# Kernel optimization log

Hardware: AMD Instinct MI355X
Metric: run time of the kernel (lower is better)

Reference implementation:

```python
import jax, jax.numpy as jnp
import numpy as np

B, S, D, H = 4, 2048, 1024, 16
DH = D // H  # head dim == module's 'scale'


def setup_inputs() -> dict:
    key = jax.random.key(0)
    ks = jax.random.split(key, 9)
    std = 1.0 / np.sqrt(D)
    return {
        "x": jax.random.normal(ks[0], (B, S, D), dtype=jnp.float32),
        "Wq": jax.random.normal(ks[1], (D, D), dtype=jnp.float32) * std,
        "bq": jax.random.normal(ks[2], (D,), dtype=jnp.float32) * std,
        "Wk": jax.random.normal(ks[3], (D, D), dtype=jnp.float32) * std,
        "bk": jax.random.normal(ks[4], (D,), dtype=jnp.float32) * std,
        "Wv": jax.random.normal(ks[5], (D, D), dtype=jnp.float32) * std,
        "bv": jax.random.normal(ks[6], (D,), dtype=jnp.float32) * std,
        "Wo": jax.random.normal(ks[7], (D, D), dtype=jnp.float32) * std,
        "bo": jax.random.normal(ks[8], (D,), dtype=jnp.float32) * std,
    }


def reference(x, Wq, bq, Wk, bk, Wv, bv, Wo, bo):
    b, s, d = x.shape
    # torch Linear: y = x @ W.T + b
    q = (x @ Wq.T + bq).reshape(b, s, H, DH).transpose(0, 2, 1, 3)  # [B,H,S,Dh]
    k = (x @ Wk.T + bk).reshape(b, s, H, DH).transpose(0, 2, 1, 3)
    v = (x @ Wv.T + bv).reshape(b, s, H, DH).transpose(0, 2, 1, 3)
    # scaled dot-product with causal mask (prefill: Tq == Tk, empty cache)
    scores = jnp.einsum("bhqd,bhkd->bhqk", q, k) / jnp.sqrt(
        jnp.asarray(DH, dtype=jnp.float32))
    causal = jnp.tril(jnp.ones((s, s), dtype=bool))  # [S,S]
    scores = jnp.where(causal, scores, jnp.asarray(-1e9, dtype=scores.dtype))
    attn = jax.nn.softmax(scores, axis=-1)
    out = jnp.einsum("bhqk,bhkd->bhqd", attn, v)  # [B,H,S,Dh]
    out = out.transpose(0, 2, 1, 3).reshape(b, s, d)
    return out @ Wo.T + bo
```

## Files before the change

kernel.cpp:

```cpp
#include <hip/hip_runtime.h>
#include <hip/hip_bf16.h>
#include <stdint.h>

#define NB 4
#define NS 2048
#define ND 1024
#define NH 16
#define NDH 64
#define NM (NB*NS)

typedef __attribute__((ext_vector_type(8))) short bf16x8;
typedef __attribute__((ext_vector_type(4))) float f32x4;
typedef __attribute__((ext_vector_type(16))) float f32x16;
typedef __attribute__((ext_vector_type(8))) unsigned short u16x8;

static __device__ __forceinline__ unsigned short f2bf(float f) {
  union { float f; unsigned u; } v; v.f = f;
  return (unsigned short)((v.u + 0x7FFFu + ((v.u >> 16) & 1u)) >> 16);
}

static __device__ __forceinline__ void gload_lds16(const void* g, void* l) {
  __builtin_amdgcn_global_load_lds(
      (__attribute__((address_space(1))) unsigned int*)(uintptr_t)g,
      (__attribute__((address_space(3))) unsigned int*)(uintptr_t)(size_t)(l),
      16, 0, 0);
}

static __device__ __forceinline__ unsigned cvtpk(float lo, float hi) {
  unsigned r;
  asm("v_cvt_pk_bf16_f32 %0, %1, %2" : "=v"(r) : "v"(lo), "v"(hi));
  return r;
}
static __device__ __forceinline__ void plswap(unsigned &a, unsigned &b) {
  asm("v_permlane32_swap_b32 %0, %1" : "+v"(a), "+v"(b));
}

__global__ void k_cvt(const float* __restrict__ src, unsigned short* __restrict__ dst, int n8) {
  int i = blockIdx.x * blockDim.x + threadIdx.x;
  if (i >= n8) return;
  const float4* s = (const float4*)src + (size_t)i * 2;
  float4 a = s[0], b = s[1];
  u16x8 o;
  o[0]=f2bf(a.x); o[1]=f2bf(a.y); o[2]=f2bf(a.z); o[3]=f2bf(a.w);
  o[4]=f2bf(b.x); o[5]=f2bf(b.y); o[6]=f2bf(b.z); o[7]=f2bf(b.w);
  *((u16x8*)dst + i) = o;
}

__global__ void k_cvtw(const float* __restrict__ s0, const float* __restrict__ s1,
                       const float* __restrict__ s2, const float* __restrict__ s3,
                       unsigned short* __restrict__ d0, unsigned short* __restrict__ d1,
                       unsigned short* __restrict__ d2, unsigned short* __restrict__ d3) {
  constexpr int NG = ND*ND/8;
  int i = blockIdx.x * blockDim.x + threadIdx.x;
  const int m = i / NG, j = i - m*NG;
  const float* src = m==0 ? s0 : (m==1 ? s1 : (m==2 ? s2 : s3));
  unsigned short* dst = m==0 ? d0 : (m==1 ? d1 : (m==2 ? d2 : d3));
  const float4* s = (const float4*)src + (size_t)j * 2;
  float4 a = s[0], b = s[1];
  u16x8 o;
  o[0]=f2bf(a.x); o[1]=f2bf(a.y); o[2]=f2bf(a.z); o[3]=f2bf(a.w);
  o[4]=f2bf(b.x); o[5]=f2bf(b.y); o[6]=f2bf(b.z); o[7]=f2bf(b.w);
  *((u16x8*)dst + j) = o;
}

__global__ __launch_bounds__(256)
void k_gemm_qkv(const unsigned short* __restrict__ A,
                const unsigned short* __restrict__ Wqp, const unsigned short* __restrict__ Wkp,
                const unsigned short* __restrict__ Wvp,
                const float* __restrict__ bqp, const float* __restrict__ bkp,
                const float* __restrict__ bvp,
                unsigned short* __restrict__ Qo, unsigned short* __restrict__ Ko,
                unsigned short* __restrict__ Vto, float qscale)
{
  constexpr int K = ND, BK = 32;
  __shared__ unsigned short Alds[128*BK];
  __shared__ unsigned short Blds[128*BK];
  const int bcf = blockIdx.x;
  const int mat = bcf >> 3, bc = bcf & 7;
  const unsigned short* W = mat==0 ? Wqp : (mat==1 ? Wkp : Wvp);
  const float* bias = mat==0 ? bqp : (mat==1 ? bkp : bvp);
  const float scale = mat==0 ? qscale : 1.0f;

  const int tid = threadIdx.x;
  const int wid = tid >> 6, lane = tid & 63;
  const int g = lane >> 4, lr = lane & 15;
  const int br = blockIdx.y;
  const int wr = (wid >> 1) << 6, wc = (wid & 1) << 6;

  f32x4 acc[4][4];
  #pragma unroll
  for (int m=0;m<4;m++)
    #pragma unroll
    for (int n=0;n<4;n++) acc[m][n] = f32x4{0.f,0.f,0.f,0.f};

  const unsigned short* Ab = A + (size_t)br*128*K;
  const unsigned short* Wb = W + (size_t)bc*128*K;
  const int r0 = tid >> 2, c0 = (tid & 3) * 8;
  const int r1 = (256 + tid) >> 2;

  for (int k0 = 0; k0 < K; k0 += BK) {
    gload_lds16(Ab + (size_t)r0*K + k0 + c0, &Alds[tid*8]);
    gload_lds16(Ab + (size_t)r1*K + k0 + c0, &Alds[(256+tid)*8]);
    gload_lds16(Wb + (size_t)r0*K + k0 + c0, &Blds[tid*8]);
    gload_lds16(Wb + (size_t)r1*K + k0 + c0, &Blds[(256+tid)*8]);
    __syncthreads();
    bf16x8 af[4], bfr[4];
    #pragma unroll
    for (int m=0;m<4;m++) af[m]  = *(const bf16x8*)&Alds[(wr + m*16 + lr)*BK + g*8];
    #pragma unroll
    for (int n=0;n<4;n++) bfr[n] = *(const bf16x8*)&Blds[(wc + n*16 + lr)*BK + g*8];
    #pragma unroll
    for (int m=0;m<4;m++)
      #pragma unroll
      for (int n=0;n<4;n++)
        acc[m][n] = __builtin_amdgcn_mfma_f32_16x16x32_bf16(af[m], bfr[n], acc[m][n], 0, 0, 0);
    __syncthreads();
  }

  #pragma unroll
  for (int m=0;m<4;m++) {
    const int rbase = br*128 + wr + m*16 + g*4;
    #pragma unroll
    for (int n=0;n<4;n++) {
      const int col = bc*128 + wc + n*16 + lr;
      const float bv = bias[col];
      #pragma unroll
      for (int j=0;j<4;j++) {
        const int row = rbase + j;
        const float val = (acc[m][n][j] + bv) * scale;
        const int b = row >> 11, s = row & (NS-1), h = col >> 6, dh = col & 63;
        if (mat == 2)
          Vto[(((size_t)b*NH + h)*NDH + dh)*NS + s] = f2bf(val);
        else
          (mat==0 ? Qo : Ko)[(((size_t)b*NH + h)*NS + s)*NDH + dh] = f2bf(val);
      }
    }
  }
}

__global__ __launch_bounds__(256)
void k_gemm_o(const unsigned short* __restrict__ A,
              const unsigned short* __restrict__ W,
              const float* __restrict__ bias,
              float* __restrict__ outp)
{
  constexpr int K = ND, BK = 32;
  __shared__ unsigned short Alds[128*BK];
  __shared__ unsigned short Blds[128*BK];
  const int tid = threadIdx.x;
  const int wid = tid >> 6, lane = tid & 63;
  const int g = lane >> 4, lr = lane & 15;
  const int bc = blockIdx.x, br = blockIdx.y;
  const int wr = (wid >> 1) << 6, wc = (wid & 1) << 6;

  f32x4 acc[4][4];
  #pragma unroll
  for (int m=0;m<4;m++)
    #pragma unroll
    for (int n=0;n<4;n++) acc[m][n] = f32x4{0.f,0.f,0.f,0.f};

  const unsigned short* Ab = A + (size_t)br*128*K;
  const unsigned short* Wb = W + (size_t)bc*128*K;
  const int r0 = tid >> 2, c0 = (tid & 3) * 8;
  const int r1 = (256 + tid) >> 2;

  for (int k0 = 0; k0 < K; k0 += BK) {
    gload_lds16(Ab + (size_t)r0*K + k0 + c0, &Alds[tid*8]);
    gload_lds16(Ab + (size_t)r1*K + k0 + c0, &Alds[(256+tid)*8]);
    gload_lds16(Wb + (size_t)r0*K + k0 + c0, &Blds[tid*8]);
    gload_lds16(Wb + (size_t)r1*K + k0 + c0, &Blds[(256+tid)*8]);
    __syncthreads();
    bf16x8 af[4], bfr[4];
    #pragma unroll
    for (int m=0;m<4;m++) af[m]  = *(const bf16x8*)&Alds[(wr + m*16 + lr)*BK + g*8];
    #pragma unroll
    for (int n=0;n<4;n++) bfr[n] = *(const bf16x8*)&Blds[(wc + n*16 + lr)*BK + g*8];
    #pragma unroll
    for (int m=0;m<4;m++)
      #pragma unroll
      for (int n=0;n<4;n++)
        acc[m][n] = __builtin_amdgcn_mfma_f32_16x16x32_bf16(af[m], bfr[n], acc[m][n], 0, 0, 0);
    __syncthreads();
  }

  #pragma unroll
  for (int m=0;m<4;m++) {
    const int rbase = br*128 + wr + m*16 + g*4;
    #pragma unroll
    for (int n=0;n<4;n++) {
      const int col = bc*128 + wc + n*16 + lr;
      const float bv = bias[col];
      #pragma unroll
      for (int j=0;j<4;j++)
        outp[(size_t)(rbase + j)*ND + col] = acc[m][n][j] + bv;
    }
  }
}

__global__ __launch_bounds__(128, 4)
void k_attn(const unsigned short* __restrict__ Qg,
            const unsigned short* __restrict__ Kg,
            const unsigned short* __restrict__ Vtg,
            unsigned short* __restrict__ Og)
{
  __shared__ unsigned short Klds[64*64];
  __shared__ unsigned short Vlds[64*64];
  __shared__ float scL[64];
  const int tid = threadIdx.x;
  const int wid = tid >> 6, lane = tid & 63;
  const int ql = lane & 31, hi = lane >> 5;
  const int bh = blockIdx.x;
  const int qt = (int)gridDim.y - 1 - (int)blockIdx.y;
  const int qbB = qt * 64;
  const int wq = qbB + wid * 32;

  const unsigned short* Qh  = Qg  + (size_t)bh*NS*NDH;
  const unsigned short* Kh  = Kg  + (size_t)bh*NS*NDH;
  const unsigned short* Vth = Vtg + (size_t)bh*NDH*NS;

  bf16x8 qf[4];
  #pragma unroll
  for (int ds=0; ds<4; ++ds)
    qf[ds] = *(const bf16x8*)(Qh + (size_t)(wq+ql)*NDH + ds*16 + hi*8);

  f32x16 acc0, acc1;
  #pragma unroll
  for (int r=0;r<16;++r) { acc0[r]=0.f; acc1[r]=0.f; }
  float lsum = 0.f;

  const int sr = tid >> 3, sc = tid & 7;
  const int swz = (sc ^ (sr & 7)) * 8;

  const int ntiles = qt + 1;
  for (int kt = 0; kt < ntiles; ++kt) {
    const int kbase = kt << 6;
    #pragma unroll
    for (int c=0;c<4;c++)
      gload_lds16(Kh + (size_t)(kbase + c*16 + sr)*NDH + swz, &Klds[(c*128+tid)*8]);
    #pragma unroll
    for (int c=0;c<4;c++)
      gload_lds16(Vth + (size_t)(c*16 + sr)*NS + kbase + swz, &Vlds[(c*128+tid)*8]);
    __syncthreads();
    #pragma unroll
    for (int h32 = 0; h32 < 2; ++h32) {
      const int kb32 = kbase + h32*32;
      if (kb32 <= wq) {
        const int krow = h32*32 + ql;
        f32x16 st;
        #pragma unroll
        for (int r=0;r<16;++r) st[r] = 0.f;
        __builtin_amdgcn_s_setprio(1);
        #pragma unroll
        for (int ds=0; ds<4; ++ds) {
          bf16x8 kf = *(const bf16x8*)&Klds[krow*64 + (((ds*2+hi) ^ (krow&7))*8)];
          st = __builtin_amdgcn_mfma_f32_32x32x16_bf16(kf, qf[ds], st, 0,0,0);
        }
        __builtin_amdgcn_s_setprio(0);
        if (kb32 == wq) {
          #pragma unroll
          for (int r=0;r<16;++r) {
            const int koff = (r&3) + 8*(r>>2) + 4*hi;
            if (koff > ql) st[r] = -1e30f;
          }
        }
        float p[16]; float ls = 0.f;
        #pragma unroll
        for (int r=0;r<16;++r) { p[r] = __builtin_amdgcn_exp2f(st[r]); ls += p[r]; }
        lsum += ls;
        unsigned w0 = cvtpk(p[0],p[1]),  w1 = cvtpk(p[2],p[3]);
        unsigned w2 = cvtpk(p[4],p[5]),  w3 = cvtpk(p[6],p[7]);
        plswap(w0, w2); plswap(w1, w3);
        unsigned z0 = cvtpk(p[8],p[9]),  z1 = cvtpk(p[10],p[11]);
        unsigned z2 = cvtpk(p[12],p[13]),z3 = cvtpk(p[14],p[15]);
        plswap(z0, z2); plswap(z1, z3);
        union { unsigned u[4]; bf16x8 v; } pk0, pk1;
        pk0.u[0]=w0; pk0.u[1]=w1; pk0.u[2]=w2; pk0.u[3]=w3;
        pk1.u[0]=z0; pk1.u[1]=z1; pk1.u[2]=z2; pk1.u[3]=z3;
        __builtin_amdgcn_s_setprio(1);
        #pragma unroll
        for (int nt=0; nt<2; ++nt) {
          const int drow = nt*32 + ql;
          #pragma unroll
          for (int ksl=0; ksl<2; ++ksl) {
            const int slot = h32*4 + ksl*2 + hi;
            bf16x8 vf = *(const bf16x8*)&Vlds[drow*64 + ((slot ^ (drow&7))*8)];
            f32x16 &a = nt ? acc1 : acc0;
            a = __builtin_amdgcn_mfma_f32_32x32x16_bf16(ksl ? pk1.v : pk0.v, vf, a, 0,0,0);
          }
        }
        __builtin_amdgcn_s_setprio(0);
      }
    }
    __syncthreads();
  }

  const float l = lsum + __shfl_xor(lsum, 32, 64);
  scL[wid*32 + ql] = 1.0f / l;
  const int b = bh >> 4, h = bh & 15;
  #pragma unroll
  for (int rq=0; rq<4; ++rq) {
    f32x4 lv = *(const f32x4*)&scL[wid*32 + rq*8 + 4*hi];
    #pragma unroll
    for (int j=0;j<4;j++) {
      const float inv = lv[j];
      const int s = wq + rq*8 + 4*hi + j;
      unsigned short* orow = Og + ((size_t)b*NS + s)*ND + h*NDH;
      orow[ql]      = f2bf(acc0[rq*4+j] * inv);
      orow[32 + ql] = f2bf(acc1[rq*4+j] * inv);
    }
  }
}

extern "C" void kernel_launch(void* const* d_in, const int* in_sizes, int n_in,
                              void* d_out, int out_size, void* d_ws, size_t ws_size,
                              hipStream_t stream) {
  (void)in_sizes; (void)n_in; (void)out_size; (void)ws_size;
  const float* x  = (const float*)d_in[0];
  const float* Wq = (const float*)d_in[1];
  const float* bq = (const float*)d_in[2];
  const float* Wk = (const float*)d_in[3];
  const float* bk = (const float*)d_in[4];
  const float* Wv = (const float*)d_in[5];
  const float* bv = (const float*)d_in[6];
  const float* Wo = (const float*)d_in[7];
  const float* bo = (const float*)d_in[8];

  char* ws = (char*)d_ws;
  unsigned short* xb  = (unsigned short*)(ws + 0);
  unsigned short* Wqb = (unsigned short*)(ws + 16777216);
  unsigned short* Wkb = (unsigned short*)(ws + 18874368);
  unsigned short* Wvb = (unsigned short*)(ws + 20971520);
  unsigned short* Wob = (unsigned short*)(ws + 23068672);
  unsigned short* Qb  = (unsigned short*)(ws + 25165824);
  unsigned short* Kb  = (unsigned short*)(ws + 41943040);
  unsigned short* Vtb = (unsigned short*)(ws + 58720256);
  unsigned short* Ob  = (unsigned short*)(ws + 75497472);

  k_cvt<<<dim3(NM*ND/8/256), dim3(256), 0, stream>>>(x, xb, NM*ND/8);
  k_cvtw<<<dim3(4*ND*ND/8/256), dim3(256), 0, stream>>>(Wq, Wk, Wv, Wo, Wqb, Wkb, Wvb, Wob);

  const float qscale = 0.125f * 1.4426950408889634f;
  k_gemm_qkv<<<dim3(24, NM/128), dim3(256), 0, stream>>>(
      xb, Wqb, Wkb, Wvb, bq, bk, bv, Qb, Kb, Vtb, qscale);

  k_attn<<<dim3(NB*NH, NS/64), dim3(128), 0, stream>>>(Qb, Kb, Vtb, Ob);

  k_gemm_o<<<dim3(ND/128, NM/128), dim3(256), 0, stream>>>(Ob, Wob, bo, (float*)d_out);
}
```

Before: 184.6 us.

## Double-buffer LDS tiles in GEMM and attention kernels to prefetch next tile

The QKV GEMM, output GEMM and attention kernels now use two LDS buffers. Each iteration issues the async global-to-LDS loads for the next K/V or K-slice tile before computing on the current one, so memory latency can overlap with MFMA work. MFMA sections in the GEMMs are also wrapped in s_setprio raises. The cost is double the LDS per block, which may lower occupancy. Correctness relies on the end-of-iteration barrier waiting for the outstanding loads.

```diff
diff --git a/kernel.cpp b/kernel.cpp
--- a/kernel.cpp
+++ b/kernel.cpp
@@ -73,8 +73,8 @@
                 unsigned short* __restrict__ Vto, float qscale)
 {
   constexpr int K = ND, BK = 32;
-  __shared__ unsigned short Alds[128*BK];
-  __shared__ unsigned short Blds[128*BK];
+  __shared__ unsigned short Alds[2][128*BK];
+  __shared__ unsigned short Blds[2][128*BK];
   const int bcf = blockIdx.x;
   const int mat = bcf >> 3, bc = bcf & 7;
   const unsigned short* W = mat==0 ? Wqp : (mat==1 ? Wkp : Wvp);
@@ -98,23 +98,32 @@
   const int r0 = tid >> 2, c0 = (tid & 3) * 8;
   const int r1 = (256 + tid) >> 2;
 
+  auto stage = [&](int b, int k0) {
+    gload_lds16(Ab + (size_t)r0*K + k0 + c0, &Alds[b][tid*8]);
+    gload_lds16(Ab + (size_t)r1*K + k0 + c0, &Alds[b][(256+tid)*8]);
+    gload_lds16(Wb + (size_t)r0*K + k0 + c0, &Blds[b][tid*8]);
+    gload_lds16(Wb + (size_t)r1*K + k0 + c0, &Blds[b][(256+tid)*8]);
+  };
+
+  stage(0, 0);
+  __syncthreads();
+  int cur = 0;
   for (int k0 = 0; k0 < K; k0 += BK) {
-    gload_lds16(Ab + (size_t)r0*K + k0 + c0, &Alds[tid*8]);
-    gload_lds16(Ab + (size_t)r1*K + k0 + c0, &Alds[(256+tid)*8]);
-    gload_lds16(Wb + (size_t)r0*K + k0 + c0, &Blds[tid*8]);
-    gload_lds16(Wb + (size_t)r1*K + k0 + c0, &Blds[(256+tid)*8]);
-    __syncthreads();
+    if (k0 + BK < K) stage(cur ^ 1, k0 + BK);
     bf16x8 af[4], bfr[4];
     #pragma unroll
-    for (int m=0;m<4;m++) af[m]  = *(const bf16x8*)&Alds[(wr + m*16 + lr)*BK + g*8];
-    #pragma unroll
-    for (int n=0;n<4;n++) bfr[n] = *(const bf16x8*)&Blds[(wc + n*16 + lr)*BK + g*8];
+    for (int m=0;m<4;m++) af[m]  = *(const bf16x8*)&Alds[cur][(wr + m*16 + lr)*BK + g*8];
+    #pragma unroll
+    for (int n=0;n<4;n++) bfr[n] = *(const bf16x8*)&Blds[cur][(wc + n*16 + lr)*BK + g*8];
+    __builtin_amdgcn_s_setprio(1);
     #pragma unroll
     for (int m=0;m<4;m++)
       #pragma unroll
       for (int n=0;n<4;n++)
         acc[m][n] = __builtin_amdgcn_mfma_f32_16x16x32_bf16(af[m], bfr[n], acc[m][n], 0, 0, 0);
+    __builtin_amdgcn_s_setprio(0);
     __syncthreads();
+    cur ^= 1;
   }
 
   #pragma unroll
@@ -145,8 +154,8 @@
               float* __restrict__ outp)
 {
   constexpr int K = ND, BK = 32;
-  __shared__ unsigned short Alds[128*BK];
-  __shared__ unsigned short Blds[128*BK];
+  __shared__ unsigned short Alds[2][128*BK];
+  __shared__ unsigned short Blds[2][128*BK];
   const int tid = threadIdx.x;
   const int wid = tid >> 6, lane = tid & 63;
   const int g = lane >> 4, lr = lane & 15;
@@ -164,23 +173,32 @@
   const int r0 = tid >> 2, c0 = (tid & 3) * 8;
   const int r1 = (256 + tid) >> 2;
 
+  auto stage = [&](int b, int k0) {
+    gload_lds16(Ab + (size_t)r0*K + k0 + c0, &Alds[b][tid*8]);
+    gload_lds16(Ab + (size_t)r1*K + k0 + c0, &Alds[b][(256+tid)*8]);
+    gload_lds16(Wb + (size_t)r0*K + k0 + c0, &Blds[b][tid*8]);
+    gload_lds16(Wb + (size_t)r1*K + k0 + c0, &Blds[b][(256+tid)*8]);
+  };
+
+  stage(0, 0);
+  __syncthreads();
+  int cur = 0;
   for (int k0 = 0; k0 < K; k0 += BK) {
-    gload_lds16(Ab + (size_t)r0*K + k0 + c0, &Alds[tid*8]);
-    gload_lds16(Ab + (size_t)r1*K + k0 + c0, &Alds[(256+tid)*8]);
-    gload_lds16(Wb + (size_t)r0*K + k0 + c0, &Blds[tid*8]);
-    gload_lds16(Wb + (size_t)r1*K + k0 + c0, &Blds[(256+tid)*8]);
-    __syncthreads();
+    if (k0 + BK < K) stage(cur ^ 1, k0 + BK);
     bf16x8 af[4], bfr[4];
     #pragma unroll
-    for (int m=0;m<4;m++) af[m]  = *(const bf16x8*)&Alds[(wr + m*16 + lr)*BK + g*8];
-    #pragma unroll
-    for (int n=0;n<4;n++) bfr[n] = *(const bf16x8*)&Blds[(wc + n*16 + lr)*BK + g*8];
+    for (int m=0;m<4;m++) af[m]  = *(const bf16x8*)&Alds[cur][(wr + m*16 + lr)*BK + g*8];
+    #pragma unroll
+    for (int n=0;n<4;n++) bfr[n] = *(const bf16x8*)&Blds[cur][(wc + n*16 + lr)*BK + g*8];
+    __builtin_amdgcn_s_setprio(1);
     #pragma unroll
     for (int m=0;m<4;m++)
       #pragma unroll
       for (int n=0;n<4;n++)
         acc[m][n] = __builtin_amdgcn_mfma_f32_16x16x32_bf16(af[m], bfr[n], acc[m][n], 0, 0, 0);
+    __builtin_amdgcn_s_setprio(0);
     __syncthreads();
+    cur ^= 1;
   }
 
   #pragma unroll
@@ -203,8 +221,8 @@
             const unsigned short* __restrict__ Vtg,
             unsigned short* __restrict__ Og)
 {
-  __shared__ unsigned short Klds[64*64];
-  __shared__ unsigned short Vlds[64*64];
+  __shared__ unsigned short Klds[2][64*64];
+  __shared__ unsigned short Vlds[2][64*64];
   __shared__ float scL[64];
   const int tid = threadIdx.x;
   const int wid = tid >> 6, lane = tid & 63;
@@ -231,16 +249,22 @@
   const int sr = tid >> 3, sc = tid & 7;
   const int swz = (sc ^ (sr & 7)) * 8;
 
+  auto stageKV = [&](int b, int kbase) {
+    #pragma unroll
+    for (int c=0;c<4;c++)
+      gload_lds16(Kh + (size_t)(kbase + c*16 + sr)*NDH + swz, &Klds[b][(c*128+tid)*8]);
+    #pragma unroll
+    for (int c=0;c<4;c++)
+      gload_lds16(Vth + (size_t)(c*16 + sr)*NS + kbase + swz, &Vlds[b][(c*128+tid)*8]);
+  };
+
   const int ntiles = qt + 1;
+  stageKV(0, 0);
+  __syncthreads();
+  int cur = 0;
   for (int kt = 0; kt < ntiles; ++kt) {
     const int kbase = kt << 6;
-    #pragma unroll
-    for (int c=0;c<4;c++)
-      gload_lds16(Kh + (size_t)(kbase + c*16 + sr)*NDH + swz, &Klds[(c*128+tid)*8]);
-    #pragma unroll
-    for (int c=0;c<4;c++)
-      gload_lds16(Vth + (size_t)(c*16 + sr)*NS + kbase + swz, &Vlds[(c*128+tid)*8]);
-    __syncthreads();
+    if (kt + 1 < ntiles) stageKV(cur ^ 1, (kt+1) << 6);
     #pragma unroll
     for (int h32 = 0; h32 < 2; ++h32) {
       const int kb32 = kbase + h32*32;
@@ -252,7 +276,7 @@
         __builtin_amdgcn_s_setprio(1);
         #pragma unroll
         for (int ds=0; ds<4; ++ds) {
-          bf16x8 kf = *(const bf16x8*)&Klds[krow*64 + (((ds*2+hi) ^ (krow&7))*8)];
+          bf16x8 kf = *(const bf16x8*)&Klds[cur][krow*64 + (((ds*2+hi) ^ (krow&7))*8)];
           st = __builtin_amdgcn_mfma_f32_32x32x16_bf16(kf, qf[ds], st, 0,0,0);
         }
         __builtin_amdgcn_s_setprio(0);
@@ -283,7 +307,7 @@
           #pragma unroll
           for (int ksl=0; ksl<2; ++ksl) {
             const int slot = h32*4 + ksl*2 + hi;
-            bf16x8 vf = *(const bf16x8*)&Vlds[drow*64 + ((slot ^ (drow&7))*8)];
+            bf16x8 vf = *(const bf16x8*)&Vlds[cur][drow*64 + ((slot ^ (drow&7))*8)];
             f32x16 &a = nt ? acc1 : acc0;
             a = __builtin_amdgcn_mfma_f32_32x32x16_bf16(ksl ? pk1.v : pk0.v, vf, a, 0,0,0);
           }
@@ -292,6 +316,7 @@
       }
     }
     __syncthreads();
+    cur ^= 1;
   }
 
   const float l = lsum + __shfl_xor(lsum, 32, 64);
```

New measurement: 190.2 us. 3.0% more time.
